# Performance work log

Measured on AMD Instinct MI355X. Metric: run time of the kernel, lower is better.

The kernel has to match this reference:

```python
import jax, jax.numpy as jnp
import numpy as np
from jax import lax

B, H, W = 256, 26, 4
LAT, QOUT = 64, 1024
K, D, Z = 4, 32, 64   # num_flows, num_ortho_vecs, z_size
STEPS = 100
BN_EPS = 1e-5


def setup_inputs():
    ks = iter(jax.random.split(jax.random.key(0), 80))
    def rn(shape, s=0.05):
        return jax.random.normal(next(ks), shape, jnp.float32) * s
    z1 = lambda n: jnp.zeros((n,), jnp.float32)
    o1 = lambda n: jnp.ones((n,), jnp.float32)
    return {
        "x": jax.random.normal(next(ks), (B, 1, H, W), jnp.float32),
        "eps": jax.random.normal(next(ks), (B, LAT), jnp.float32),
        "cw1": rn((32, 1, 3, 4)), "cb1": z1(32), "g1": o1(32), "be1": z1(32),
        "cw2": rn((16, 32, 5, 1)), "cb2": z1(16), "g2": o1(16), "be2": z1(16),
        "cw3": rn((8, 16, 7, 1)), "cb3": z1(8), "g3": o1(8), "be3": z1(8),
        "d1_w": rn((112, QOUT)), "d1_b": z1(QOUT), "bn1_g": o1(QOUT), "bn1_b": z1(QOUT),
        "mu_w": rn((QOUT, LAT)), "mu_b": z1(LAT),
        "lv_w": rn((QOUT, LAT)), "lv_b": z1(LAT),
        "ad_w": rn((QOUT, K * D * D)), "ad_b": z1(K * D * D),
        "adg1_w": rn((QOUT, K * D)), "adg1_b": z1(K * D),
        "adg2_w": rn((QOUT, K * D)), "adg2_b": z1(K * D),
        "aq_w": rn((QOUT, K * Z * D)), "aq_b": rn((K * Z * D,), 0.05),
        "ab_w": rn((QOUT, K * D)), "ab_b": z1(K * D),
        "d3_w": rn((LAT, QOUT)), "d3_b": z1(QOUT), "bn3_g": o1(QOUT), "bn3_b": z1(QOUT),
        "d4_w": rn((QOUT, 112)), "d4_b": z1(112), "bn4_g": o1(112), "bn4_b": z1(112),
        "tw1": rn((8, 16, 7, 1)), "tb1": z1(16), "tg1": o1(16), "tbe1": z1(16),
        "tw2": rn((16, 32, 5, 1)), "tb2": z1(32), "tg2": o1(32), "tbe2": z1(32),
        "tw3": rn((32, 1, 3, 4)), "tb3": z1(1),
    }


def _conv(x, w, b):
    y = lax.conv_general_dilated(x, w, (1, 1), 'VALID',
                                 dimension_numbers=('NCHW', 'OIHW', 'NCHW'))
    return y + b[None, :, None, None]


def _tconv(x, w, b):
    # torch ConvTranspose2d weight layout (in, out, kH, kW) == OIHW of the
    # forward conv being transposed -> transpose_kernel=True matches torch.
    y = lax.conv_transpose(x, w, (1, 1), 'VALID',
                           dimension_numbers=('NCHW', 'OIHW', 'NCHW'),
                           transpose_kernel=True)
    return y + b[None, :, None, None]


def _bn2d(x, g, b):  # BatchNorm2d, training mode (biased batch stats)
    m = x.mean((0, 2, 3), keepdims=True)
    v = ((x - m) ** 2).mean((0, 2, 3), keepdims=True)
    return (x - m) * lax.rsqrt(v + BN_EPS) * g[None, :, None, None] + b[None, :, None, None]


def _bn1d(x, g, b):  # BatchNorm1d, training mode
    m = x.mean(0)
    v = ((x - m) ** 2).mean(0)
    return (x - m) * lax.rsqrt(v + BN_EPS) * g + b


def reference(x, eps, cw1, cb1, g1, be1, cw2, cb2, g2, be2, cw3, cb3, g3, be3,
              d1_w, d1_b, bn1_g, bn1_b, mu_w, mu_b, lv_w, lv_b,
              ad_w, ad_b, adg1_w, adg1_b, adg2_w, adg2_b, aq_w, aq_b, ab_w, ab_b,
              d3_w, d3_b, bn3_g, bn3_b, d4_w, d4_b, bn4_g, bn4_b,
              tw1, tb1, tg1, tbe1, tw2, tb2, tg2, tbe2, tw3, tb3):
    # ---- encoder CNN ----
    h = jax.nn.relu(_bn2d(_conv(x, cw1, cb1), g1, be1))
    h = jax.nn.relu(_bn2d(_conv(h, cw2, cb2), g2, be2))
    h = jax.nn.relu(_bn2d(_conv(h, cw3, cb3), g3, be3))   # (B,8,14,1)
    out = h.reshape(B, -1)                                 # (B,112)
    out = jax.nn.relu(_bn1d(out @ d1_w + d1_b, bn1_g, bn1_b))
    mean = out @ mu_w + mu_b
    logvar = out @ lv_w + lv_b
    # ---- amortized flow parameters ----
    full_d = (out @ ad_w + ad_b).reshape(B, D, D, K)
    diag1 = jnp.tanh(out @ adg1_w + adg1_b).reshape(B, D, K)
    diag2 = jnp.tanh(out @ adg2_w + adg2_b).reshape(B, D, K)
    triu = jnp.triu(jnp.ones((D, D), x.dtype), 1)[None, :, :, None]
    di = jnp.arange(D)
    r1 = (full_d * triu).at[:, di, di, :].set(diag1)
    r2 = (jnp.transpose(full_d, (0, 2, 1, 3)) * triu).at[:, di, di, :].set(diag2)
    q = out @ aq_w + aq_b                                  # (B, K*Z*D)
    bflow = (out @ ab_w + ab_b).reshape(B, 1, D, K)
    # ---- Bjorck orthogonalization (100 fixed-point steps) ----
    qn = q.reshape(B * K, Z * D)
    qn = qn / jnp.linalg.norm(qn, axis=1, keepdims=True)
    amat = qn.reshape(B * K, Z, D)
    eye = jnp.eye(D, dtype=x.dtype)
    @jax.checkpoint
    def step(a, _):
        gram = jnp.einsum('nzd,nze->nde', a, a)            # a^T a, (N,D,D)
        a = jnp.einsum('nzd,nde->nze', a, eye + 0.5 * (eye - gram))
        return a, None
    amat, _ = lax.scan(step, amat, None, length=STEPS)
    q_ortho = amat.reshape(B, K, Z, D).transpose(1, 0, 2, 3)  # (K,B,Z,D)
    # ---- reparameterize + Sylvester flows ----
    z0 = mean + eps * jnp.exp(0.5 * logvar)
    z = z0
    ldj = jnp.zeros((B,), x.dtype)
    for k in range(K):
        r1k, r2k, qk, bk = r1[..., k], r2[..., k], q_ortho[k], bflow[..., k]
        qr2 = jnp.einsum('bzd,bed->bze', qk, r2k)          # q @ r2^T (B,Z,D)
        qr1 = jnp.einsum('bzd,bde->bze', qk, r1k)          # q @ r1   (B,Z,D)
        r2qzb = jnp.einsum('bz,bzd->bd', z, qr2)[:, None, :] + bk  # (B,1,D)
        z = jnp.einsum('bod,bzd->boz', jnp.tanh(r2qzb), qr1)[:, 0, :] + z
        dr1 = r1k[:, di, di]
        dr2 = r2k[:, di, di]
        diag_j = (1.0 - jnp.tanh(r2qzb) ** 2)[:, 0, :] * (dr1 * dr2) + 1.0
        ldj = ldj + jnp.log(jnp.abs(diag_j)).sum(-1)
    # ---- decoder ----
    d = jax.nn.relu(_bn1d(z @ d3_w + d3_b, bn3_g, bn3_b))
    d = jax.nn.relu(_bn1d(d @ d4_w + d4_b, bn4_g, bn4_b))
    d = d.reshape(B, 8, 14, 1)
    d = jax.nn.relu(_bn2d(_tconv(d, tw1, tb1), tg1, tbe1))
    d = jax.nn.relu(_bn2d(_tconv(d, tw2, tb2), tg2, tbe2))
    x_dec = _tconv(d, tw3, tb3)
    return (x_dec, mean, logvar, ldj, z0, z)
```

## Files before the change

### kernel.cpp

```cpp
#include <hip/hip_runtime.h>
#include <math.h>

#define NS_STEPS 30

typedef __attribute__((ext_vector_type(8))) _Float16 half8;
typedef __attribute__((ext_vector_type(4))) _Float16 half4v;
typedef __attribute__((ext_vector_type(8))) short short8;
typedef __attribute__((ext_vector_type(4))) float floatx4;

static __device__ inline unsigned short f2bf(float f) {
  union { float f; unsigned u; } v; v.f = f;
  unsigned r = v.u + 0x7fffu + ((v.u >> 16) & 1u);
  return (unsigned short)(r >> 16);
}
static __device__ inline float bf2f(unsigned short h) {
  union { unsigned u; float f; } v; v.u = ((unsigned)h) << 16;
  return v.f;
}

__global__ __launch_bounds__(256) void conv1_k(const float* __restrict__ x,
    const float* __restrict__ w, const float* __restrict__ bias,
    float* __restrict__ out) {
  __shared__ float ws[384];
  int tid = threadIdx.x;
  for (int i = tid; i < 384; i += 256) ws[i] = w[i];
  __syncthreads();
  int idx = blockIdx.x * 256 + tid;
  if (idx >= 196608) return;
  int b = idx / 768, r = idx % 768;
  int c = r / 24, h = r % 24;
  const float* xb = x + b * 104 + h * 4;
  const float* wc = ws + c * 12;
  float acc = bias[c];
  #pragma unroll
  for (int kh = 0; kh < 3; kh++) {
    #pragma unroll
    for (int kw = 0; kw < 4; kw++)
      acc += xb[kh * 4 + kw] * wc[kh * 4 + kw];
  }
  out[idx] = acc;
}

__global__ __launch_bounds__(256) void conv2_k(const float* __restrict__ in,
    const float* __restrict__ w, const float* __restrict__ bias,
    float* __restrict__ out) {
  __shared__ float ws[2560];
  int tid = threadIdx.x;
  for (int i = tid; i < 2560; i += 256) ws[i] = w[i];
  __syncthreads();
  int idx = blockIdx.x * 256 + tid;
  if (idx >= 81920) return;
  int b = idx / 320, r = idx % 320;
  int c = r / 20, h = r % 20;
  const float* ib = in + b * 768 + h;
  const float* wc = ws + c * 160;
  float acc = bias[c];
  for (int i = 0; i < 32; i++) {
    #pragma unroll
    for (int kh = 0; kh < 5; kh++)
      acc += ib[i * 24 + kh] * wc[i * 5 + kh];
  }
  out[idx] = acc;
}

__global__ __launch_bounds__(256) void conv3_k(const float* __restrict__ in,
    const float* __restrict__ w, const float* __restrict__ bias,
    float* __restrict__ out) {
  __shared__ float ws[896];
  int tid = threadIdx.x;
  for (int i = tid; i < 896; i += 256) ws[i] = w[i];
  __syncthreads();
  int idx = blockIdx.x * 256 + tid;
  if (idx >= 28672) return;
  int b = idx / 112, r = idx % 112;
  int c = r / 14, h = r % 14;
  const float* ib = in + b * 320 + h;
  const float* wc = ws + c * 112;
  float acc = bias[c];
  for (int i = 0; i < 16; i++) {
    #pragma unroll
    for (int kh = 0; kh < 7; kh++)
      acc += ib[i * 20 + kh] * wc[i * 7 + kh];
  }
  out[idx] = acc;
}

__global__ __launch_bounds__(256) void tconv1_k(const float* __restrict__ in,
    const float* __restrict__ w, const float* __restrict__ bias,
    float* __restrict__ out) {
  __shared__ float ws[896];
  int tid = threadIdx.x;
  for (int i = tid; i < 896; i += 256) ws[i] = w[i];
  __syncthreads();
  int idx = blockIdx.x * 256 + tid;
  if (idx >= 81920) return;
  int b = idx / 320, r = idx % 320;
  int c = r / 20, s = r % 20;
  float acc = bias[c];
  for (int o = 0; o < 8; o++) {
    #pragma unroll
    for (int kh = 0; kh < 7; kh++) {
      int hs = s - kh;
      if (hs >= 0 && hs < 14)
        acc += in[b * 112 + o * 14 + hs] * ws[o * 112 + c * 7 + kh];
    }
  }
  out[idx] = acc;
}

__global__ __launch_bounds__(256) void tconv2_k(const float* __restrict__ in,
    const float* __restrict__ w, const float* __restrict__ bias,
    float* __restrict__ out) {
  __shared__ float ws[2560];
  int tid = threadIdx.x;
  for (int i = tid; i < 2560; i += 256) ws[i] = w[i];
  __syncthreads();
  int idx = blockIdx.x * 256 + tid;
  if (idx >= 196608) return;
  int b = idx / 768, r = idx % 768;
  int c = r / 24, s = r % 24;
  float acc = bias[c];
  for (int o = 0; o < 16; o++) {
    #pragma unroll
    for (int kh = 0; kh < 5; kh++) {
      int hs = s - kh;
      if (hs >= 0 && hs < 20)
        acc += in[b * 320 + o * 20 + hs] * ws[o * 160 + c * 5 + kh];
    }
  }
  out[idx] = acc;
}

__global__ __launch_bounds__(256) void tconv3_k(const float* __restrict__ in,
    const float* __restrict__ w, const float* __restrict__ bias,
    float* __restrict__ out) {
  __shared__ float ws[384];
  int tid = threadIdx.x;
  for (int i = tid; i < 384; i += 256) ws[i] = w[i];
  __syncthreads();
  int idx = blockIdx.x * 256 + tid;
  if (idx >= 26624) return;
  int b = idx / 104, r = idx % 104;
  int sh = r / 4, sw = r % 4;
  float acc = bias[0];
  for (int o = 0; o < 32; o++) {
    #pragma unroll
    for (int kh = 0; kh < 3; kh++) {
      int hs = sh - kh;
      if (hs >= 0 && hs < 24)
        acc += in[b * 768 + o * 24 + hs] * ws[o * 12 + kh * 4 + sw];
    }
  }
  out[idx] = acc;
}

__global__ __launch_bounds__(256) void bn2d_k(float* __restrict__ x,
    const float* __restrict__ g, const float* __restrict__ be,
    int C, int HW) {
  __shared__ float rs[256], rs2[256];
  int c = blockIdx.x, tid = threadIdx.x;
  int total = 256 * HW;
  float s = 0.f, s2 = 0.f;
  for (int i = tid; i < total; i += 256) {
    int b = i / HW, j = i - b * HW;
    float v = x[(b * C + c) * HW + j];
    s += v; s2 += v * v;
  }
  rs[tid] = s; rs2[tid] = s2;
  __syncthreads();
  for (int off = 128; off > 0; off >>= 1) {
    if (tid < off) { rs[tid] += rs[tid + off]; rs2[tid] += rs2[tid + off]; }
    __syncthreads();
  }
  float m = rs[0] / (float)total;
  float var = rs2[0] / (float)total - m * m;
  float rstd = rsqrtf(var + 1e-5f) * g[c];
  float bb = be[c];
  for (int i = tid; i < total; i += 256) {
    int b = i / HW, j = i - b * HW;
    size_t idx = (size_t)(b * C + c) * HW + j;
    float v = (x[idx] - m) * rstd + bb;
    x[idx] = v > 0.f ? v : 0.f;
  }
}

__global__ __launch_bounds__(256) void bn1d_k(float* __restrict__ x,
    const float* __restrict__ g, const float* __restrict__ be, int N) {
  __shared__ float p1[8][32], p2[8][32];
  int t = threadIdx.x;
  int cl = t & 31, rg = t >> 5;
  int c = blockIdx.x * 32 + cl;
  float s = 0.f, s2 = 0.f;
  if (c < N) {
    for (int r = rg * 32; r < rg * 32 + 32; r++) {
      float v = x[r * N + c];
      s += v; s2 += v * v;
    }
  }
  p1[rg][cl] = s; p2[rg][cl] = s2;
  __syncthreads();
  float ts = 0.f, ts2 = 0.f;
  #pragma unroll
  for (int i = 0; i < 8; i++) { ts += p1[i][cl]; ts2 += p2[i][cl]; }
  float m = ts * (1.f / 256.f);
  float var = ts2 * (1.f / 256.f) - m * m;
  float rstd = rsqrtf(var + 1e-5f) * ((c < N) ? g[c] : 1.f);
  float bb = (c < N) ? be[c] : 0.f;
  if (c < N) {
    for (int r = rg * 32; r < rg * 32 + 32; r++) {
      float v = (x[r * N + c] - m) * rstd + bb;
      x[r * N + c] = v > 0.f ? v : 0.f;
    }
  }
}

__global__ __launch_bounds__(256) void gemm_os_k(const float* __restrict__ A,
    const float* __restrict__ W, const float* __restrict__ bias,
    float* __restrict__ C, int K, int N) {
  __shared__ float As[112 * 68];
  __shared__ float Bs[112 * 68];
  int tid = threadIdx.x;
  int nb = blockIdx.x, mb = blockIdx.y;
  int K16 = K >> 4;
  {
    int row = tid >> 2;
    const float* Ar = A + (size_t)(mb * 64 + row) * K;
    for (int i = 0; i < K16; i++) {
      int j = (tid & 3) + 4 * i;
      float4 v = *(const float4*)(Ar + j * 4);
      int k = j * 4;
      As[k * 68 + row] = v.x;
      As[(k + 1) * 68 + row] = v.y;
      As[(k + 2) * 68 + row] = v.z;
      As[(k + 3) * 68 + row] = v.w;
    }
  }
  {
    int n4 = (tid & 15) * 4;
    for (int i = 0; i < K16; i++) {
      int k = (tid >> 4) + 16 * i;
      float4 v = *(const float4*)(W + (size_t)k * N + nb * 64 + n4);
      *(float4*)(Bs + k * 68 + n4) = v;
    }
  }
  __syncthreads();
  int tm = tid >> 4, tn = tid & 15;
  int m0 = tm * 4, n0 = tn * 4;
  float acc[4][4] = {{0.f}};
  #pragma unroll 8
  for (int kk = 0; kk < K; kk++) {
    float4 a = *(const float4*)(As + kk * 68 + m0);
    float4 b = *(const float4*)(Bs + kk * 68 + n0);
    acc[0][0] += a.x*b.x; acc[0][1] += a.x*b.y; acc[0][2] += a.x*b.z; acc[0][3] += a.x*b.w;
    acc[1][0] += a.y*b.x; acc[1][1] += a.y*b.y; acc[1][2] += a.y*b.z; acc[1][3] += a.y*b.w;
    acc[2][0] += a.z*b.x; acc[2][1] += a.z*b.y; acc[2][2] += a.z*b.z; acc[2][3] += a.z*b.w;
    acc[3][0] += a.w*b.x; acc[3][1] += a.w*b.y; acc[3][2] += a.w*b.z; acc[3][3] += a.w*b.w;
  }
  #pragma unroll
  for (int i = 0; i < 4; i++) {
    int m = mb * 64 + m0 + i;
    #pragma unroll
    for (int j = 0; j < 4; j++) {
      int n = nb * 64 + n0 + j;
      C[(size_t)m * N + n] = acc[i][j] + bias[n];
    }
  }
}

__global__ __launch_bounds__(256) void gemm_ks_k(const float* __restrict__ A,
    const float* __restrict__ W, const float* __restrict__ bias,
    float* __restrict__ C) {
  __shared__ float As[64 * 68];
  __shared__ float Bs[64 * 68];
  int tid = threadIdx.x;
  int nb = blockIdx.x, mb = blockIdx.y, kc = blockIdx.z;
  int k0 = kc * 64;
  {
    int row = tid >> 2;
    const float* Ar = A + (size_t)(mb * 64 + row) * 1024 + k0;
    #pragma unroll
    for (int i = 0; i < 4; i++) {
      int j = (tid & 3) + 4 * i;
      float4 v = *(const float4*)(Ar + j * 4);
      int k = j * 4;
      As[k * 68 + row] = v.x;
      As[(k + 1) * 68 + row] = v.y;
      As[(k + 2) * 68 + row] = v.z;
      As[(k + 3) * 68 + row] = v.w;
    }
  }
  {
    int n4 = (tid & 15) * 4;
    int nbase = nb * 64 + n4;
    #pragma unroll
    for (int i = 0; i < 4; i++) {
      int k = (tid >> 4) + 16 * i;
      const float* Wr = W + (size_t)(k0 + k) * 112;
      float4 v;
      v.x = (nbase     < 112) ? Wr[nbase]     : 0.f;
      v.y = (nbase + 1 < 112) ? Wr[nbase + 1] : 0.f;
      v.z = (nbase + 2 < 112) ? Wr[nbase + 2] : 0.f;
      v.w = (nbase + 3 < 112) ? Wr[nbase + 3] : 0.f;
      *(float4*)(Bs + k * 68 + n4) = v;
    }
  }
  __syncthreads();
  int tm = tid >> 4, tn = tid & 15;
  int m0 = tm * 4, n0 = tn * 4;
  float acc[4][4] = {{0.f}};
  #pragma unroll 8
  for (int kk = 0; kk < 64; kk++) {
    float4 a = *(const float4*)(As + kk * 68 + m0);
    float4 b = *(const float4*)(Bs + kk * 68 + n0);
    acc[0][0] += a.x*b.x; acc[0][1] += a.x*b.y; acc[0][2] += a.x*b.z; acc[0][3] += a.x*b.w;
    acc[1][0] += a.y*b.x; acc[1][1] += a.y*b.y; acc[1][2] += a.y*b.z; acc[1][3] += a.y*b.w;
    acc[2][0] += a.z*b.x; acc[2][1] += a.z*b.y; acc[2][2] += a.z*b.z; acc[2][3] += a.z*b.w;
    acc[3][0] += a.w*b.x; acc[3][1] += a.w*b.y; acc[3][2] += a.w*b.z; acc[3][3] += a.w*b.w;
  }
  #pragma unroll
  for (int i = 0; i < 4; i++) {
    int m = mb * 64 + m0 + i;
    #pragma unroll
    for (int j = 0; j < 4; j++) {
      int n = nb * 64 + n0 + j;
      if (n < 112) {
        float v = acc[i][j] + (kc == 0 ? bias[n] : 0.f);
        atomicAdd(&C[m * 112 + n], v);
      }
    }
  }
}

struct HeadArgs {
  const float* W[7];
  const float* b[7];
  float* dst[7];
  int off[8];
  int ldw[7];
  int op[7];
};

__global__ __launch_bounds__(256) void heads_mfma_k(const float* __restrict__ A,
                                                    HeadArgs ha) {
  __shared__ short Ah[64 * 36], Al[64 * 36], Wh[64 * 36], Wl[64 * 36];
  int tid = threadIdx.x;
  int nb = blockIdx.x, mb = blockIdx.y;
  int r = 0;
  int gc = nb * 64;
  while (gc >= ha.off[r + 1]) r++;
  const float* Wp = ha.W[r];
  const float* bias = ha.b[r];
  float* dst = ha.dst[r];
  int ldw = ha.ldw[r];
  int op = ha.op[r];
  int nloc0 = gc - ha.off[r];

  int w = tid >> 6, l = tid & 63;
  int lane16 = l & 15, quad = l >> 4;
  int am = tid >> 2, ac = (tid & 3) * 8;
  const float* Arow = A + (mb * 64 + am) * 1024 + ac;
  int kr = tid >> 3, wc = (tid & 7) * 8;
  const float* Wrow = Wp + nloc0 + wc;

  const floatx4 zero4 = {0.f, 0.f, 0.f, 0.f};
  floatx4 acc[4] = {zero4, zero4, zero4, zero4};

  for (int chunk = 0; chunk < 32; ++chunk) {
    int k0 = chunk * 32;
    float4 a0 = *(const float4*)(Arow + k0);
    float4 a1 = *(const float4*)(Arow + k0 + 4);
    float4 w0 = *(const float4*)(Wrow + (k0 + kr) * ldw);
    float4 w1 = *(const float4*)(Wrow + (k0 + kr) * ldw + 4);
    __syncthreads();
    {
      float av[8] = {a0.x,a0.y,a0.z,a0.w,a1.x,a1.y,a1.z,a1.w};
      short hi[8], lo[8];
      #pragma unroll
      for (int i = 0; i < 8; i++) {
        unsigned short h = f2bf(av[i]);
        hi[i] = (short)h;
        lo[i] = (short)f2bf(av[i] - bf2f(h));
      }
      #pragma unroll
      for (int i = 0; i < 8; i++) {
        Ah[am * 36 + ac + i] = hi[i];
        Al[am * 36 + ac + i] = lo[i];
      }
      float wv[8] = {w0.x,w0.y,w0.z,w0.w,w1.x,w1.y,w1.z,w1.w};
      #pragma unroll
      for (int i = 0; i < 8; i++) {
        unsigned short h = f2bf(wv[i]);
        Wh[(wc + i) * 36 + kr] = (short)h;
        Wl[(wc + i) * 36 + kr] = (short)f2bf(wv[i] - bf2f(h));
      }
    }
    __syncthreads();
    short8 bh = *(short8*)(Wh + (w * 16 + lane16) * 36 + quad * 8);
    short8 bl = *(short8*)(Wl + (w * 16 + lane16) * 36 + quad * 8);
    #pragma unroll
    for (int mt = 0; mt < 4; mt++) {
      short8 ah = *(short8*)(Ah + (mt * 16 + lane16) * 36 + quad * 8);
      short8 al = *(short8*)(Al + (mt * 16 + lane16) * 36 + quad * 8);
      acc[mt] = __builtin_amdgcn_mfma_f32_16x16x32_bf16(ah, bh, acc[mt], 0, 0, 0);
      acc[mt] = __builtin_amdgcn_mfma_f32_16x16x32_bf16(ah, bl, acc[mt], 0, 0, 0);
      acc[mt] = __builtin_amdgcn_mfma_f32_16x16x32_bf16(al, bh, acc[mt], 0, 0, 0);
    }
  }
  int n = nloc0 + w * 16 + lane16;
  float bv = bias[n];
  #pragma unroll
  for (int mt = 0; mt < 4; mt++) {
    #pragma unroll
    for (int i = 0; i < 4; i++) {
      int m = mb * 64 + mt * 16 + quad * 4 + i;
      float v = acc[mt][i] + bv;
      if (op == 1) v = tanhf(v);
      dst[m * ldw + n] = v;
    }
  }
}

__global__ __launch_bounds__(64) void ns_f16split_k(const float* __restrict__ q,
                                                    float* __restrict__ amat) {
  __align__(16) __shared__ _Float16 arena[12288];
  int l = threadIdx.x;
  int lane16 = l & 15, quad = l >> 4;
  _Float16* Ah_cm = arena;
  _Float16* Al_cm = arena + 2304;
  _Float16* Mh_cm = arena + 4608;
  _Float16* Ml_cm = arena + 5888;
  _Float16* Ah_rm = arena + 7168;
  _Float16* Al_rm = arena + 9728;
  float* Afin = (float*)arena;

  const float* g = q + (size_t)blockIdx.x * 2048;
  float* o = amat + (size_t)blockIdx.x * 2048;

  float vals[32];
  float ss = 0.f;
  #pragma unroll
  for (int j = 0; j < 8; j++) {
    float4 v = *(const float4*)(g + l * 32 + j * 4);
    vals[4*j] = v.x; vals[4*j+1] = v.y; vals[4*j+2] = v.z; vals[4*j+3] = v.w;
    ss += v.x*v.x + v.y*v.y + v.z*v.z + v.w*v.w;
  }
  #pragma unroll
  for (int off = 32; off > 0; off >>= 1) ss += __shfl_xor(ss, off);
  float rn = rsqrtf(ss);
  #pragma unroll
  for (int i = 0; i < 32; i++) vals[i] *= rn;
  #pragma unroll
  for (int j = 0; j < 8; j++) {
    half4v ph, pl;
    #pragma unroll
    for (int r = 0; r < 4; r++) {
      float v = vals[4*j + r];
      _Float16 h = (_Float16)v;
      _Float16 lo = (_Float16)(v - (float)h);
      ph[r] = h; pl[r] = lo;
    }
    *(half4v*)(Ah_rm + l * 40 + j * 4) = ph;
    *(half4v*)(Al_rm + l * 40 + j * 4) = pl;
  }
  #pragma unroll
  for (int i = 0; i < 32; i++) {
    float v = vals[i];
    _Float16 h = (_Float16)v;
    Ah_cm[i * 72 + l] = h;
    Al_cm[i * 72 + l] = (_Float16)(v - (float)h);
  }
  __syncthreads();

  const floatx4 zero4 = {0.f, 0.f, 0.f, 0.f};
  for (int s = 0; s < NS_STEPS; s++) {
    bool last = (s == NS_STEPS - 1);
    half8 fah[2][2], fal[2][2];
    #pragma unroll
    for (int ti = 0; ti < 2; ti++)
      #pragma unroll
      for (int c = 0; c < 2; c++) {
        fah[ti][c] = *(half8*)(Ah_cm + (ti * 16 + lane16) * 72 + c * 32 + quad * 8);
        fal[ti][c] = *(half8*)(Al_cm + (ti * 16 + lane16) * 72 + c * 32 + quad * 8);
      }
    floatx4 gf[2][2] = {{zero4, zero4}, {zero4, zero4}};
    #pragma unroll
    for (int ti = 0; ti < 2; ti++)
      #pragma unroll
      for (int tj = 0; tj < 2; tj++)
        #pragma unroll
        for (int c = 0; c < 2; c++) {
          gf[ti][tj] = __builtin_amdgcn_mfma_f32_16x16x32_f16(
              fah[ti][c], fah[tj][c], gf[ti][tj], 0, 0, 0);
          gf[ti][tj] = __builtin_amdgcn_mfma_f32_16x16x32_f16(
              fah[ti][c], fal[tj][c], gf[ti][tj], 0, 0, 0);
          gf[ti][tj] = __builtin_amdgcn_mfma_f32_16x16x32_f16(
              fal[ti][c], fah[tj][c], gf[ti][tj], 0, 0, 0);
        }
    #pragma unroll
    for (int ti = 0; ti < 2; ti++)
      #pragma unroll
      for (int tj = 0; tj < 2; tj++) {
        int col = tj * 16 + lane16;
        int row0 = ti * 16 + quad * 4;
        half4v ph, pl;
        #pragma unroll
        for (int r = 0; r < 4; r++) {
          float m = ((row0 + r) == col ? 1.5f : 0.f) - 0.5f * gf[ti][tj][r];
          _Float16 h = (_Float16)m;
          ph[r] = h; pl[r] = (_Float16)(m - (float)h);
        }
        *(half4v*)(Mh_cm + col * 40 + row0) = ph;
        *(half4v*)(Ml_cm + col * 40 + row0) = pl;
      }
    __syncthreads();
    half8 fmh[2], fml[2], fbh[4], fbl[4];
    #pragma unroll
    for (int ti = 0; ti < 2; ti++) {
      fmh[ti] = *(half8*)(Mh_cm + (ti * 16 + lane16) * 40 + quad * 8);
      fml[ti] = *(half8*)(Ml_cm + (ti * 16 + lane16) * 40 + quad * 8);
    }
    #pragma unroll
    for (int tj = 0; tj < 4; tj++) {
      fbh[tj] = *(half8*)(Ah_rm + (tj * 16 + lane16) * 40 + quad * 8);
      fbl[tj] = *(half8*)(Al_rm + (tj * 16 + lane16) * 40 + quad * 8);
    }
    floatx4 df[2][4];
    #pragma unroll
    for (int ti = 0; ti < 2; ti++)
      #pragma unroll
      for (int tj = 0; tj < 4; tj++) {
        df[ti][tj] = __builtin_amdgcn_mfma_f32_16x16x32_f16(
            fmh[ti], fbh[tj], zero4, 0, 0, 0);
        df[ti][tj] = __builtin_amdgcn_mfma_f32_16x16x32_f16(
            fmh[ti], fbl[tj], df[ti][tj], 0, 0, 0);
        df[ti][tj] = __builtin_amdgcn_mfma_f32_16x16x32_f16(
            fml[ti], fbh[tj], df[ti][tj], 0, 0, 0);
      }
    __syncthreads();
    if (!last) {
      #pragma unroll
      for (int ti = 0; ti < 2; ti++)
        #pragma unroll
        for (int tj = 0; tj < 4; tj++) {
          int z = tj * 16 + lane16;
          int d0 = ti * 16 + quad * 4;
          half4v ph, pl;
          #pragma unroll
          for (int r = 0; r < 4; r++) {
            float v = df[ti][tj][r];
            _Float16 h = (_Float16)v;
            ph[r] = h; pl[r] = (_Float16)(v - (float)h);
          }
          *(half4v*)(Ah_rm + z * 40 + d0) = ph;
          *(half4v*)(Al_rm + z * 40 + d0) = pl;
          #pragma unroll
          for (int r = 0; r < 4; r++) {
            Ah_cm[(d0 + r) * 72 + z] = ph[r];
            Al_cm[(d0 + r) * 72 + z] = pl[r];
          }
        }
    } else {
      #pragma unroll
      for (int ti = 0; ti < 2; ti++)
        #pragma unroll
        for (int tj = 0; tj < 4; tj++) {
          int z = tj * 16 + lane16;
          int d0 = ti * 16 + quad * 4;
          float4 v;
          v.x = df[ti][tj][0]; v.y = df[ti][tj][1];
          v.z = df[ti][tj][2]; v.w = df[ti][tj][3];
          *(float4*)(Afin + z * 36 + d0) = v;
        }
    }
    __syncthreads();
  }
  #pragma unroll
  for (int j = 0; j < 8; j++) {
    int f = j * 256 + l * 4;
    int z = f >> 5, d = f & 31;
    float4 v = *(const float4*)(Afin + z * 36 + d);
    *(float4*)(o + f) = v;
  }
}

__global__ __launch_bounds__(64) void flow_k(const float* __restrict__ amat,
    const float* __restrict__ fd, const float* __restrict__ dg1,
    const float* __restrict__ dg2, const float* __restrict__ ab,
    const float* __restrict__ eps, float* __restrict__ dout) {
  __shared__ float Ps[32][64];
  __shared__ float wsh[32], tsh[32], ush[32];
  int b = blockIdx.x, l = threadIdx.x;
  float mv  = dout[26624 + b * 64 + l];
  float lvv = dout[43008 + b * 64 + l];
  float z0 = mv + eps[b * 64 + l] * expf(0.5f * lvv);
  dout[59648 + b * 64 + l] = z0;
  float zv = z0;
  float ldj = 0.f;
  float q[32];
  for (int k = 0; k < 4; k++) {
    const float4* qrow = (const float4*)(amat + (size_t)(b * 4 + k) * 2048 + l * 32);
    #pragma unroll
    for (int j = 0; j < 8; j++) {
      float4 v = qrow[j];
      q[4*j] = v.x; q[4*j+1] = v.y; q[4*j+2] = v.z; q[4*j+3] = v.w;
    }
    #pragma unroll
    for (int d = 0; d < 32; d++) Ps[d][l] = zv * q[d];
    __syncthreads();
    if (l < 32) {
      const float4* pr = (const float4*)Ps[l];
      float s = 0.f;
      #pragma unroll
      for (int j = 0; j < 16; j++) {
        float4 v = pr[j];
        s += v.x + v.y + v.z + v.w;
      }
      wsh[l] = s;
    }
    __syncthreads();
    if (l < 32) {
      int e = l;
      float acc = ab[b * 128 + e * 4 + k] + wsh[e] * dg2[b * 128 + e * 4 + k];
      for (int d = e + 1; d < 32; d++)
        acc += wsh[d] * fd[b * 4096 + d * 128 + e * 4 + k];
      float tt = tanhf(acc);
      tsh[e] = tt;
      float dd = (1.f - tt * tt) * (dg1[b*128 + e*4 + k] * dg2[b*128 + e*4 + k]) + 1.f;
      ldj += logf(fabsf(dd));
    }
    __syncthreads();
    if (l < 32) {
      int d = l;
      float acc = tsh[d] * dg1[b * 128 + d * 4 + k];
      for (int e = d + 1; e < 32; e++)
        acc += fd[b * 4096 + d * 128 + e * 4 + k] * tsh[e];
      ush[d] = acc;
    }
    __syncthreads();
    #pragma unroll
    for (int d = 0; d < 32; d++) zv += q[d] * ush[d];
    __syncthreads();
  }
  dout[76032 + b * 64 + l] = zv;
  for (int off = 16; off > 0; off >>= 1) ldj += __shfl_down(ldj, off, 32);
  if (l == 0) dout[59392 + b] = ldj;
}

extern "C" void kernel_launch(void* const* d_in, const int* in_sizes, int n_in,
                              void* d_out, int out_size, void* d_ws, size_t ws_size,
                              hipStream_t stream) {
  (void)in_sizes; (void)n_in; (void)out_size; (void)ws_size;
  const float* x     = (const float*)d_in[0];
  const float* eps   = (const float*)d_in[1];
  const float* cw1   = (const float*)d_in[2];
  const float* cb1   = (const float*)d_in[3];
  const float* g1    = (const float*)d_in[4];
  const float* be1   = (const float*)d_in[5];
  const float* cw2   = (const float*)d_in[6];
  const float* cb2   = (const float*)d_in[7];
  const float* g2    = (const float*)d_in[8];
  const float* be2   = (const float*)d_in[9];
  const float* cw3   = (const float*)d_in[10];
  const float* cb3   = (const float*)d_in[11];
  const float* g3    = (const float*)d_in[12];
  const float* be3   = (const float*)d_in[13];
  const float* d1_w  = (const float*)d_in[14];
  const float* d1_b  = (const float*)d_in[15];
  const float* bn1_g = (const float*)d_in[16];
  const float* bn1_b = (const float*)d_in[17];
  const float* mu_w  = (const float*)d_in[18];
  const float* mu_b  = (const float*)d_in[19];
  const float* lv_w  = (const float*)d_in[20];
  const float* lv_b  = (const float*)d_in[21];
  const float* ad_w  = (const float*)d_in[22];
  const float* ad_b  = (const float*)d_in[23];
  const float* adg1_w= (const float*)d_in[24];
  const float* adg1_b= (const float*)d_in[25];
  const float* adg2_w= (const float*)d_in[26];
  const float* adg2_b= (const float*)d_in[27];
  const float* aq_w  = (const float*)d_in[28];
  const float* aq_b  = (const float*)d_in[29];
  const float* ab_w  = (const float*)d_in[30];
  const float* ab_b  = (const float*)d_in[31];
  const float* d3_w  = (const float*)d_in[32];
  const float* d3_b  = (const float*)d_in[33];
  const float* bn3_g = (const float*)d_in[34];
  const float* bn3_b = (const float*)d_in[35];
  const float* d4_w  = (const float*)d_in[36];
  const float* d4_b  = (const float*)d_in[37];
  const float* bn4_g = (const float*)d_in[38];
  const float* bn4_b = (const float*)d_in[39];
  const float* tw1   = (const float*)d_in[40];
  const float* tb1   = (const float*)d_in[41];
  const float* tg1   = (const float*)d_in[42];
  const float* tbe1  = (const float*)d_in[43];
  const float* tw2   = (const float*)d_in[44];
  const float* tb2   = (const float*)d_in[45];
  const float* tg2   = (const float*)d_in[46];
  const float* tbe2  = (const float*)d_in[47];
  const float* tw3   = (const float*)d_in[48];
  const float* tb3   = (const float*)d_in[49];

  float* out = (float*)d_out;
  float* wsf = (float*)d_ws;
  float* h1   = wsf;
  float* h2   = wsf + 196608;
  float* h3   = wsf + 278528;
  float* out1 = wsf + 307200;
  float* fd   = wsf + 569344;
  float* dg1  = wsf + 1617920;
  float* dg2  = wsf + 1650688;
  float* qb   = wsf + 1683456;
  float* ab   = wsf + 3780608;
  float* amat = wsf + 3813376;
  float* dec1 = out1;
  float* dec2 = h3;
  float* t1   = h2;
  float* t2   = h1;

  float* mean_o = out + 26624;
  float* lv_o   = out + 43008;
  float* z_o    = out + 76032;

  conv1_k<<<768, 256, 0, stream>>>(x, cw1, cb1, h1);
  bn2d_k<<<32, 256, 0, stream>>>(h1, g1, be1, 32, 24);
  conv2_k<<<320, 256, 0, stream>>>(h1, cw2, cb2, h2);
  bn2d_k<<<16, 256, 0, stream>>>(h2, g2, be2, 16, 20);
  conv3_k<<<112, 256, 0, stream>>>(h2, cw3, cb3, h3);
  bn2d_k<<<8, 256, 0, stream>>>(h3, g3, be3, 8, 14);

  gemm_os_k<<<dim3(16, 4), 256, 0, stream>>>(h3, d1_w, d1_b, out1, 112, 1024);
  bn1d_k<<<32, 256, 0, stream>>>(out1, bn1_g, bn1_b, 1024);

  HeadArgs ha;
  ha.W[0] = mu_w;   ha.b[0] = mu_b;   ha.dst[0] = mean_o; ha.ldw[0] = 64;   ha.op[0] = 0;
  ha.W[1] = lv_w;   ha.b[1] = lv_b;   ha.dst[1] = lv_o;   ha.ldw[1] = 64;   ha.op[1] = 0;
  ha.W[2] = ad_w;   ha.b[2] = ad_b;   ha.dst[2] = fd;     ha.ldw[2] = 4096; ha.op[2] = 0;
  ha.W[3] = adg1_w; ha.b[3] = adg1_b; ha.dst[3] = dg1;    ha.ldw[3] = 128;  ha.op[3] = 1;
  ha.W[4] = adg2_w; ha.b[4] = adg2_b; ha.dst[4] = dg2;    ha.ldw[4] = 128;  ha.op[4] = 1;
  ha.W[5] = aq_w;   ha.b[5] = aq_b;   ha.dst[5] = qb;     ha.ldw[5] = 8192; ha.op[5] = 0;
  ha.W[6] = ab_w;   ha.b[6] = ab_b;   ha.dst[6] = ab;     ha.ldw[6] = 128;  ha.op[6] = 0;
  ha.off[0] = 0;    ha.off[1] = 64;   ha.off[2] = 128;  ha.off[3] = 4224;
  ha.off[4] = 4352; ha.off[5] = 4480; ha.off[6] = 12672; ha.off[7] = 12800;
  heads_mfma_k<<<dim3(200, 4), 256, 0, stream>>>(out1, ha);

  ns_f16split_k<<<1024, 64, 0, stream>>>(qb, amat);
  flow_k<<<256, 64, 0, stream>>>(amat, fd, dg1, dg2, ab, eps, out);

  gemm_os_k<<<dim3(16, 4), 256, 0, stream>>>(z_o, d3_w, d3_b, dec1, 64, 1024);
  bn1d_k<<<32, 256, 0, stream>>>(dec1, bn3_g, bn3_b, 1024);
  hipMemsetAsync(dec2, 0, 28672 * sizeof(float), stream);
  gemm_ks_k<<<dim3(2, 4, 16), 256, 0, stream>>>(dec1, d4_w, d4_b, dec2);
  bn1d_k<<<4, 256, 0, stream>>>(dec2, bn4_g, bn4_b, 112);

  tconv1_k<<<320, 256, 0, stream>>>(dec2, tw1, tb1, t1);
  bn2d_k<<<16, 256, 0, stream>>>(t1, tg1, tbe1, 16, 20);
  tconv2_k<<<768, 256, 0, stream>>>(t1, tw2, tb2, t2);
  bn2d_k<<<32, 256, 0, stream>>>(t2, tg2, tbe2, 32, 24);
  tconv3_k<<<104, 256, 0, stream>>>(t2, tw3, tb3, out);
}
```

Before: 536.7 us.

## Pre-split activations into MFMA-fragment bf16 layout and double-buffer weight tiles

A new kernel converts the BN'd hidden activations once into hi/lo bf16 pairs, stored in the exact per-lane MFMA fragment order, so the heads GEMM loads A fragments straight from global memory. Previously each of the 200 column blocks redid that split for every tile. The heads kernel also double-buffers the weight tile in shared memory with register prefetch two chunks ahead, which cuts the loop to one barrier per chunk. This adds one extra launch and scratch traffic, and it aliases scratch memory over h1/h2, which are assumed dead by then.

```diff
diff --git a/kernel.cpp b/kernel.cpp
--- a/kernel.cpp
+++ b/kernel.cpp
@@ -331,6 +331,30 @@
   }
 }
 
+__global__ __launch_bounds__(256) void prep_a_k(const float* __restrict__ A,
+    short* __restrict__ ahi, short* __restrict__ alo) {
+  int gi = blockIdx.x * 256 + threadIdx.x;
+  int lane = gi & 63;
+  int t = gi >> 6;
+  int mt = t & 3; t >>= 2;
+  int c = t & 31; int mb = t >> 5;
+  int row = mb * 64 + mt * 16 + (lane & 15);
+  int k0 = c * 32 + (lane >> 4) * 8;
+  const float* src = A + (size_t)row * 1024 + k0;
+  float4 v0 = *(const float4*)(src);
+  float4 v1 = *(const float4*)(src + 4);
+  float av[8] = {v0.x, v0.y, v0.z, v0.w, v1.x, v1.y, v1.z, v1.w};
+  short8 h, lo;
+  #pragma unroll
+  for (int i = 0; i < 8; i++) {
+    unsigned short hh = f2bf(av[i]);
+    h[i] = (short)hh;
+    lo[i] = (short)f2bf(av[i] - bf2f(hh));
+  }
+  *(short8*)(ahi + (size_t)gi * 8) = h;
+  *(short8*)(alo + (size_t)gi * 8) = lo;
+}
+
 struct HeadArgs {
   const float* W[7];
   const float* b[7];
@@ -340,9 +364,10 @@
   int op[7];
 };
 
-__global__ __launch_bounds__(256) void heads_mfma_k(const float* __restrict__ A,
+__global__ __launch_bounds__(256) void heads_mfma_k(const short* __restrict__ ahi,
+                                                    const short* __restrict__ alo,
                                                     HeadArgs ha) {
-  __shared__ short Ah[64 * 36], Al[64 * 36], Wh[64 * 36], Wl[64 * 36];
+  __shared__ __align__(16) short Wsh[2][2][2048];
   int tid = threadIdx.x;
   int nb = blockIdx.x, mb = blockIdx.y;
   int r = 0;
@@ -357,55 +382,77 @@
 
   int w = tid >> 6, l = tid & 63;
   int lane16 = l & 15, quad = l >> 4;
-  int am = tid >> 2, ac = (tid & 3) * 8;
-  const float* Arow = A + (mb * 64 + am) * 1024 + ac;
-  int kr = tid >> 3, wc = (tid & 7) * 8;
-  const float* Wrow = Wp + nloc0 + wc;
+
+  int c64 = tid & 63, q4 = tid >> 6;
+  const float* wcol = Wp + (size_t)q4 * 8 * ldw + nloc0 + c64;
+  int wg = ((c64 >> 4) * 64 + q4 * 16 + (c64 & 15)) * 8;
+
+  const short* agh = ahi + (size_t)mb * 65536;
+  const short* agl = alo + (size_t)mb * 65536;
 
   const floatx4 zero4 = {0.f, 0.f, 0.f, 0.f};
   floatx4 acc[4] = {zero4, zero4, zero4, zero4};
 
-  for (int chunk = 0; chunk < 32; ++chunk) {
-    int k0 = chunk * 32;
-    float4 a0 = *(const float4*)(Arow + k0);
-    float4 a1 = *(const float4*)(Arow + k0 + 4);
-    float4 w0 = *(const float4*)(Wrow + (k0 + kr) * ldw);
-    float4 w1 = *(const float4*)(Wrow + (k0 + kr) * ldw + 4);
-    __syncthreads();
-    {
-      float av[8] = {a0.x,a0.y,a0.z,a0.w,a1.x,a1.y,a1.z,a1.w};
-      short hi[8], lo[8];
+  float wreg[8];
+  short8 whi, wlo;
+
+  #pragma unroll
+  for (int j = 0; j < 8; j++) wreg[j] = wcol[(size_t)j * ldw];
+  #pragma unroll
+  for (int j = 0; j < 8; j++) {
+    unsigned short hh = f2bf(wreg[j]);
+    whi[j] = (short)hh;
+    wlo[j] = (short)f2bf(wreg[j] - bf2f(hh));
+  }
+  *(short8*)(&Wsh[0][0][wg]) = whi;
+  *(short8*)(&Wsh[0][1][wg]) = wlo;
+  #pragma unroll
+  for (int j = 0; j < 8; j++) wreg[j] = wcol[(size_t)(32 + j) * ldw];
+  __syncthreads();
+  #pragma unroll
+  for (int j = 0; j < 8; j++) {
+    unsigned short hh = f2bf(wreg[j]);
+    whi[j] = (short)hh;
+    wlo[j] = (short)f2bf(wreg[j] - bf2f(hh));
+  }
+
+  for (int ch = 0; ch < 32; ++ch) {
+    int p = ch & 1;
+    if (ch < 31) {
+      *(short8*)(&Wsh[p ^ 1][0][wg]) = whi;
+      *(short8*)(&Wsh[p ^ 1][1][wg]) = wlo;
+    }
+    if (ch < 30) {
       #pragma unroll
-      for (int i = 0; i < 8; i++) {
-        unsigned short h = f2bf(av[i]);
-        hi[i] = (short)h;
-        lo[i] = (short)f2bf(av[i] - bf2f(h));
+      for (int j = 0; j < 8; j++)
+        wreg[j] = wcol[(size_t)((ch + 2) * 32 + j) * ldw];
+    }
+    short8 bh = *(const short8*)(&Wsh[p][0][(w * 64 + l) * 8]);
+    short8 bl = *(const short8*)(&Wsh[p][1][(w * 64 + l) * 8]);
+    short8 ah[4], al4[4];
+    #pragma unroll
+    for (int mt = 0; mt < 4; mt++) {
+      size_t ao = (size_t)ch * 2048 + mt * 512 + l * 8;
+      ah[mt]  = *(const short8*)(agh + ao);
+      al4[mt] = *(const short8*)(agl + ao);
+    }
+    #pragma unroll
+    for (int mt = 0; mt < 4; mt++) {
+      acc[mt] = __builtin_amdgcn_mfma_f32_16x16x32_bf16(ah[mt], bh, acc[mt], 0, 0, 0);
+      acc[mt] = __builtin_amdgcn_mfma_f32_16x16x32_bf16(ah[mt], bl, acc[mt], 0, 0, 0);
+      acc[mt] = __builtin_amdgcn_mfma_f32_16x16x32_bf16(al4[mt], bh, acc[mt], 0, 0, 0);
+    }
+    if (ch < 30) {
+      #pragma unroll
+      for (int j = 0; j < 8; j++) {
+        unsigned short hh = f2bf(wreg[j]);
+        whi[j] = (short)hh;
+        wlo[j] = (short)f2bf(wreg[j] - bf2f(hh));
       }
-      #pragma unroll
-      for (int i = 0; i < 8; i++) {
-        Ah[am * 36 + ac + i] = hi[i];
-        Al[am * 36 + ac + i] = lo[i];
-      }
-      float wv[8] = {w0.x,w0.y,w0.z,w0.w,w1.x,w1.y,w1.z,w1.w};
-      #pragma unroll
-      for (int i = 0; i < 8; i++) {
-        unsigned short h = f2bf(wv[i]);
-        Wh[(wc + i) * 36 + kr] = (short)h;
-        Wl[(wc + i) * 36 + kr] = (short)f2bf(wv[i] - bf2f(h));
-      }
-    }
-    __syncthreads();
-    short8 bh = *(short8*)(Wh + (w * 16 + lane16) * 36 + quad * 8);
-    short8 bl = *(short8*)(Wl + (w * 16 + lane16) * 36 + quad * 8);
-    #pragma unroll
-    for (int mt = 0; mt < 4; mt++) {
-      short8 ah = *(short8*)(Ah + (mt * 16 + lane16) * 36 + quad * 8);
-      short8 al = *(short8*)(Al + (mt * 16 + lane16) * 36 + quad * 8);
-      acc[mt] = __builtin_amdgcn_mfma_f32_16x16x32_bf16(ah, bh, acc[mt], 0, 0, 0);
-      acc[mt] = __builtin_amdgcn_mfma_f32_16x16x32_bf16(ah, bl, acc[mt], 0, 0, 0);
-      acc[mt] = __builtin_amdgcn_mfma_f32_16x16x32_bf16(al, bh, acc[mt], 0, 0, 0);
-    }
-  }
+    }
+    __syncthreads();
+  }
+
   int n = nloc0 + w * 16 + lane16;
   float bv = bias[n];
   #pragma unroll
@@ -415,7 +462,7 @@
       int m = mb * 64 + mt * 16 + quad * 4 + i;
       float v = acc[mt][i] + bv;
       if (op == 1) v = tanhf(v);
-      dst[m * ldw + n] = v;
+      dst[(size_t)m * ldw + n] = v;
     }
   }
 }
@@ -718,6 +765,9 @@
   float* t1   = h2;
   float* t2   = h1;
 
+  short* ahi = (short*)wsf;
+  short* alo = ahi + 262144;
+
   float* mean_o = out + 26624;
   float* lv_o   = out + 43008;
   float* z_o    = out + 76032;
@@ -731,6 +781,8 @@
 
   gemm_os_k<<<dim3(16, 4), 256, 0, stream>>>(h3, d1_w, d1_b, out1, 112, 1024);
   bn1d_k<<<32, 256, 0, stream>>>(out1, bn1_g, bn1_b, 1024);
+
+  prep_a_k<<<128, 256, 0, stream>>>(out1, ahi, alo);
 
   HeadArgs ha;
   ha.W[0] = mu_w;   ha.b[0] = mu_b;   ha.dst[0] = mean_o; ha.ldw[0] = 64;   ha.op[0] = 0;
@@ -742,7 +794,7 @@
   ha.W[6] = ab_w;   ha.b[6] = ab_b;   ha.dst[6] = ab;     ha.ldw[6] = 128;  ha.op[6] = 0;
   ha.off[0] = 0;    ha.off[1] = 64;   ha.off[2] = 128;  ha.off[3] = 4224;
   ha.off[4] = 4352; ha.off[5] = 4480; ha.off[6] = 12672; ha.off[7] = 12800;
-  heads_mfma_k<<<dim3(200, 4), 256, 0, stream>>>(out1, ha);
+  heads_mfma_k<<<dim3(200, 4), 256, 0, stream>>>(ahi, alo, ha);
 
   ns_f16split_k<<<1024, 64, 0, stream>>>(qb, amat);
   flow_k<<<256, 64, 0, stream>>>(amat, fd, dg1, dg2, ab, eps, out);
```

Result: faster. 521.2 us (-2.9%).
